# Optimization experiments

Hardware: AMD Instinct MI355X
Metric: run time of the kernel (lower is better)

The kernel has to match this reference:

```python
import jax, jax.numpy as jnp
import numpy as np

WIN = 9
PAD = WIN // 2
ALPHA = 0.1
BETA = 0.1
EPS_NCC = 1e-5
EPS_SC = 1e-5


def box_sum(x):
    """All-ones WIN^3 box-filter local sum, stride 1, pad WIN//2.
    Implemented separably (3 1-D convs) -- mathematically identical to the
    original single F.conv3d with a ones [1,1,9,9,9] kernel, far cheaper.
    x: [N, 1, D, H, W]"""
    for axis in range(3):
        kshape = [1, 1, 1, 1, 1]
        kshape[2 + axis] = WIN
        kern = jnp.ones(kshape, x.dtype)
        pad = [(0, 0), (0, 0), (0, 0)]
        pad[axis] = (PAD, PAD)
        x = jax.lax.conv_general_dilated(x, kern, (1, 1, 1), pad)
    return x


def setup_inputs() -> dict:
    key = jax.random.key(0)
    k1, k2, k3, k4, k5 = jax.random.split(key, 5)
    B, T, D, H, W = 1, 4, 128, 128, 128
    image = jax.random.normal(k1, (B, T, D, H, W), jnp.float32)
    mask = jax.random.uniform(k2, (B, T, D, H, W), jnp.float32)
    pred_image = jax.random.normal(k3, (B, T, D, H, W), jnp.float32)
    pred_mask = jax.random.uniform(k4, (B, T, D, H, W), jnp.float32)
    flow = jax.random.normal(k5, (T - 1, B, 3, D, H, W), jnp.float32)
    time_diff = jnp.arange(B * T, dtype=jnp.float32).reshape(B, T)
    return {"image": image, "mask": mask, "pred_image": pred_image,
            "pred_mask": pred_mask, "flow": flow, "time_diff": time_diff}


def reference(image, mask, pred_image, pred_mask, flow, time_diff):
    B, T, D, H, W = image.shape
    win_size = WIN ** 3

    # ---- NCC loss: fixed frame (t=0) vs each predicted frame t=1..T-1 ----
    # Per-t (1 - mean(cc_t)) averaged over T-1 equals 1 - mean over the
    # stacked batch since every cc_t has identical shape.
    I = jnp.broadcast_to(image[:, :1], (B, T - 1, D, H, W)).reshape(B * (T - 1), 1, D, H, W)
    J = pred_image[:, 1:].reshape(B * (T - 1), 1, D, H, W)
    I_sum = box_sum(I)
    J_sum = box_sum(J)
    I2_sum = box_sum(I * I)
    J2_sum = box_sum(J * J)
    IJ_sum = box_sum(I * J)
    u_I = I_sum / win_size
    u_J = J_sum / win_size
    cross = IJ_sum - u_J * I_sum - u_I * J_sum + u_I * u_J * win_size
    I_var = I2_sum - 2 * u_I * I_sum + u_I * u_I * win_size
    J_var = J2_sum - 2 * u_J * J_sum + u_J * u_J * win_size
    cc = cross * cross / (I_var * J_var + EPS_NCC)
    ncc = 1.0 - jnp.mean(cc)

    # ---- gradient (flow smoothness) loss, l2 penalty ----
    # flow: [T-1, B, 3, D, H, W]; per-t means of equal-shaped diffs average
    # to the global mean over the leading t axis.
    dy = jnp.square(jnp.abs(flow[:, :, :, 1:, :, :] - flow[:, :, :, :-1, :, :]))
    dx = jnp.square(jnp.abs(flow[:, :, :, :, 1:, :] - flow[:, :, :, :, :-1, :]))
    dz = jnp.square(jnp.abs(flow[:, :, :, :, :, 1:] - flow[:, :, :, :, :, :-1]))
    grad_loss = (jnp.mean(dx) + jnp.mean(dy) + jnp.mean(dz)) / 3.0

    # ---- temporal volume smoothness constraint ----
    area = jnp.sum(pred_mask, axis=(2, 3, 4)).T  # [T, B]
    area = area / jnp.max(area)
    scs = []
    for i in range(T - 2):
        for j in range(i + 1, T - 1):
            for k in range(j + 1, T):
                lam = (time_diff[:, j] - time_diff[:, i] + EPS_SC) / (
                    time_diff[:, k] - time_diff[:, i] + EPS_SC)
                scs.append(jnp.square(area[j] - area[i] - lam * (area[k] - area[i])))
    sc = jnp.mean(jnp.stack(scs, axis=1))

    return ncc + ALPHA * grad_loss + BETA * sc
```

## Files before the change

kernel.cpp:

```cpp
#include <hip/hip_runtime.h>

#define V3 (128 * 128 * 128)

__device__ __forceinline__ float block_reduce(float v, float* sm) {
#pragma unroll
  for (int off = 32; off > 0; off >>= 1) v += __shfl_down(v, off, 64);
  int lane = threadIdx.x & 63;
  int wid  = threadIdx.x >> 6;
  if (lane == 0) sm[wid] = v;
  __syncthreads();
  float r = 0.f;
  if ((int)threadIdx.x < (int)(blockDim.x >> 6)) r = sm[threadIdx.x];
  if (wid == 0) {
#pragma unroll
    for (int off = 4; off > 0; off >>= 1) r += __shfl_down(r, off, 64);
  }
  __syncthreads();
  return r;
}

__global__ __launch_bounds__(256) void area_kernel(const float* __restrict__ pm,
                                                   float* __restrict__ acc) {
  __shared__ float sm[8];
  const int t = blockIdx.y;
  const float* p = pm + (size_t)t * V3;
  const int n4 = V3 / 4;
  float s = 0.f;
  for (int i = blockIdx.x * blockDim.x + threadIdx.x; i < n4;
       i += gridDim.x * blockDim.x) {
    float4 a = *(const float4*)(p + 4 * (size_t)i);
    s += (a.x + a.y) + (a.z + a.w);
  }
  s = block_reduce(s, sm);
  if (threadIdx.x == 0) atomicAdd(acc + t, s);
}

__global__ __launch_bounds__(256) void grad_kernel(const float* __restrict__ fl,
                                                   float* __restrict__ acc) {
  __shared__ float sm[8];
  const int w4 = threadIdx.x & 31;
  const int hl = threadIdx.x >> 5;
  const int h  = blockIdx.x * 8 + hl;
  const int d0 = blockIdx.y * 16;
  const int c  = blockIdx.z;
  const float* p = fl + (size_t)c * V3 + (size_t)h * 128 + w4 * 4;
  const bool hv = (h < 127);

  float s = 0.f;
  float4 cur  = *(const float4*)(p + (size_t)d0 * 16384);
  float4 curh = hv ? *(const float4*)(p + (size_t)d0 * 16384 + 128) : cur;

#pragma unroll
  for (int dd = 0; dd < 16; ++dd) {
    const int d = d0 + dd;
    const bool dv = (d < 127);
    float4 nxt = cur, nxth = curh;
    if (dv) {
      nxt = *(const float4*)(p + (size_t)(d + 1) * 16384);
      if (hv) nxth = *(const float4*)(p + (size_t)(d + 1) * 16384 + 128);
    }
    float x;
    x = cur.y - cur.x; s += x * x;
    x = cur.z - cur.y; s += x * x;
    x = cur.w - cur.z; s += x * x;
    float nx = __shfl_down(cur.x, 1, 64);
    if (w4 != 31) { x = nx - cur.w; s += x * x; }
    if (hv) {
      x = curh.x - cur.x; s += x * x;
      x = curh.y - cur.y; s += x * x;
      x = curh.z - cur.z; s += x * x;
      x = curh.w - cur.w; s += x * x;
    }
    if (dv) {
      x = nxt.x - cur.x; s += x * x;
      x = nxt.y - cur.y; s += x * x;
      x = nxt.z - cur.z; s += x * x;
      x = nxt.w - cur.w; s += x * x;
    }
    cur = nxt; curh = nxth;
  }
  s = block_reduce(s, sm);
  if (threadIdx.x == 0) atomicAdd(acc, s);
}

template <bool WITH_I>
__global__ __launch_bounds__(256) void n1_kernel(const float* __restrict__ I0,
                                                 const float* __restrict__ Jall,
                                                 float* __restrict__ FI,
                                                 float* __restrict__ FJall) {
  constexpr int NF = WITH_I ? 5 : 3;
  __shared__ float sI[2][2][136];
  __shared__ float sJ[2][2][136];
  __shared__ float ring[2][9][NF][128];

  const int tz = blockIdx.z;
  const float* J = Jall + (size_t)tz * V3;
  float* FJ = FJall + (size_t)tz * 3 * (size_t)V3;

  const int w  = threadIdx.x & 127;
  const int dl = threadIdx.x >> 7;
  const int d  = blockIdx.y * 2 + dl;
  const int h0 = blockIdx.x * 16;
  const float* Ib = I0 + (size_t)d * 16384;
  const float* Jb = J  + (size_t)d * 16384;

#pragma unroll
  for (int sl = 0; sl < 9; ++sl)
#pragma unroll
    for (int f = 0; f < NF; ++f) ring[dl][sl][f][w] = 0.f;

  float S[NF];
#pragma unroll
  for (int f = 0; f < NF; ++f) S[f] = 0.f;

  for (int hh = h0 - 4; hh < h0 + 20; ++hh) {
    const int buf = hh & 1;
    const bool valid = (hh >= 0) && (hh < 128);
    if (valid) {
      sI[dl][buf][4 + w] = Ib[hh * 128 + w];
      sJ[dl][buf][4 + w] = Jb[hh * 128 + w];
      if (w < 4)    { sI[dl][buf][w] = 0.f;     sJ[dl][buf][w] = 0.f; }
      if (w >= 124) { sI[dl][buf][w + 8] = 0.f; sJ[dl][buf][w + 8] = 0.f; }
    }
    __syncthreads();

    float Wn[NF];
#pragma unroll
    for (int f = 0; f < NF; ++f) Wn[f] = 0.f;
    if (valid) {
#pragma unroll
      for (int k = 0; k < 9; ++k) {
        float a = sI[dl][buf][w + k];
        float b = sJ[dl][buf][w + k];
        if (WITH_I) {
          Wn[0] += a; Wn[1] += a * a;
          Wn[2] += b; Wn[3] += b * b; Wn[4] += a * b;
        } else {
          Wn[0] += b; Wn[1] += b * b; Wn[2] += a * b;
        }
      }
    }

    const int slot = (hh + 36) % 9;
#pragma unroll
    for (int f = 0; f < NF; ++f) {
      float old = ring[dl][slot][f][w];
      ring[dl][slot][f][w] = Wn[f];
      S[f] += Wn[f] - old;
    }

    const int ho = hh - 4;
    if (ho >= h0) {
      size_t base = (size_t)d * 16384 + (size_t)ho * 128 + w;
      if (WITH_I) {
        FI[base]                  = S[0];
        FI[(size_t)V3 + base]     = S[1];
        FJ[base]                  = S[2];
        FJ[(size_t)V3 + base]     = S[3];
        FJ[2 * (size_t)V3 + base] = S[4];
      } else {
        FJ[base]                  = S[0];
        FJ[(size_t)V3 + base]     = S[1];
        FJ[2 * (size_t)V3 + base] = S[2];
      }
    }
  }
}

__global__ __launch_bounds__(256) void n2_kernel(const float* __restrict__ FI,
                                                 const float* __restrict__ FJall,
                                                 float* __restrict__ acc) {
  __shared__ float sm[8];
  const float* FJ = FJall + (size_t)blockIdx.z * 3 * (size_t)V3;
  const int w  = threadIdx.x & 127;
  const int h  = blockIdx.x * 2 + (threadIdx.x >> 7);
  const int d0 = blockIdx.y * 16;
  const int hw = h * 128 + w;

  const float* P0 = FI;
  const float* P1 = FI + (size_t)V3;
  const float* P2 = FJ;
  const float* P3 = FJ + (size_t)V3;
  const float* P4 = FJ + 2 * (size_t)V3;

  float S0 = 0.f, S1 = 0.f, S2 = 0.f, S3 = 0.f, S4 = 0.f;
#pragma unroll
  for (int k = 0; k < 9; ++k) {
    int dd = d0 - 4 + k;
    bool v = (dd >= 0) && (dd < 128);
    size_t a = (size_t)(v ? dd : 0) * 16384 + hw;
    S0 += v ? P0[a] : 0.f;
    S1 += v ? P1[a] : 0.f;
    S2 += v ? P2[a] : 0.f;
    S3 += v ? P3[a] : 0.f;
    S4 += v ? P4[a] : 0.f;
  }

  const float inv_win = 1.0f / 729.0f;
  float accv = 0.f;
#pragma unroll 4
  for (int d = d0; d < d0 + 16; ++d) {
    float cross = S4 - S0 * S2 * inv_win;
    float Ivar  = S1 - S0 * S0 * inv_win;
    float Jvar  = S3 - S2 * S2 * inv_win;
    accv += cross * cross / (Ivar * Jvar + 1e-5f);

    int da = d + 5, ds = d - 4;
    bool va = da < 128, vs = ds >= 0;
    size_t aa = (size_t)(va ? da : 0) * 16384 + hw;
    size_t as = (size_t)(vs ? ds : 0) * 16384 + hw;
    S0 += (va ? P0[aa] : 0.f) - (vs ? P0[as] : 0.f);
    S1 += (va ? P1[aa] : 0.f) - (vs ? P1[as] : 0.f);
    S2 += (va ? P2[aa] : 0.f) - (vs ? P2[as] : 0.f);
    S3 += (va ? P3[aa] : 0.f) - (vs ? P3[as] : 0.f);
    S4 += (va ? P4[aa] : 0.f) - (vs ? P4[as] : 0.f);
  }

  accv = block_reduce(accv, sm);
  if (threadIdx.x == 0) atomicAdd(acc, accv);
}

__global__ void final_kernel(const float* __restrict__ ws,
                             const float* __restrict__ td,
                             float* __restrict__ out) {
  if (threadIdx.x != 0 || blockIdx.x != 0) return;
  float area[4];
  float amax = -1e30f;
#pragma unroll
  for (int t = 0; t < 4; ++t) {
    area[t] = ws[t];
    amax = fmaxf(amax, area[t]);
  }
  float a[4];
#pragma unroll
  for (int t = 0; t < 4; ++t) a[t] = area[t] / amax;

  float sc = 0.f;
  int cnt = 0;
  for (int i = 0; i < 2; ++i)
    for (int j = i + 1; j < 3; ++j)
      for (int k = j + 1; k < 4; ++k) {
        float lam = (td[j] - td[i] + 1e-5f) / (td[k] - td[i] + 1e-5f);
        float e = a[j] - a[i] - lam * (a[k] - a[i]);
        sc += e * e;
        ++cnt;
      }
  sc /= (float)cnt;

  float ncc  = 1.0f - ws[7] / (3.0f * (float)V3);
  float grad = ws[4] / (3.0f * 9.0f * 127.0f * 128.0f * 128.0f);
  out[0] = ncc + 0.1f * grad + 0.1f * sc;
}

extern "C" void kernel_launch(void* const* d_in, const int* in_sizes, int n_in,
                              void* d_out, int out_size, void* d_ws, size_t ws_size,
                              hipStream_t stream) {
  const float* image      = (const float*)d_in[0];
  const float* pred_image = (const float*)d_in[2];
  const float* pred_mask  = (const float*)d_in[3];
  const float* flow       = (const float*)d_in[4];
  const float* time_diff  = (const float*)d_in[5];
  float* out = (float*)d_out;
  float* wsf = (float*)d_ws;
  float* FI  = wsf + 64;
  float* FJ  = FI + 2 * (size_t)V3;

  hipMemsetAsync(d_ws, 0, 256, stream);

  hipLaunchKernelGGL(area_kernel, dim3(512, 4), dim3(256), 0, stream,
                     pred_mask, wsf);
  hipLaunchKernelGGL(grad_kernel, dim3(16, 8, 9), dim3(256), 0, stream,
                     flow, wsf + 4);

  const size_t need_fused = (64 + 11 * (size_t)V3) * sizeof(float);
  if (ws_size >= need_fused) {
    hipLaunchKernelGGL((n1_kernel<true>), dim3(8, 64, 1), dim3(256), 0, stream,
                       image, pred_image + (size_t)V3, FI, FJ);
    hipLaunchKernelGGL((n1_kernel<false>), dim3(8, 64, 2), dim3(256), 0, stream,
                       image, pred_image + 2 * (size_t)V3, FI,
                       FJ + 3 * (size_t)V3);
    hipLaunchKernelGGL(n2_kernel, dim3(64, 8, 3), dim3(256), 0, stream,
                       FI, FJ, wsf + 7);
  } else {
    for (int t = 0; t < 3; ++t) {
      const float* J = pred_image + (size_t)(t + 1) * V3;
      if (t == 0) {
        hipLaunchKernelGGL((n1_kernel<true>), dim3(8, 64, 1), dim3(256), 0,
                           stream, image, J, FI, FJ);
      } else {
        hipLaunchKernelGGL((n1_kernel<false>), dim3(8, 64, 1), dim3(256), 0,
                           stream, image, J, FI, FJ);
      }
      hipLaunchKernelGGL(n2_kernel, dim3(64, 8, 1), dim3(256), 0, stream,
                         FI, FJ, wsf + 7);
    }
  }

  hipLaunchKernelGGL(final_kernel, dim3(1), dim3(1), 0, stream,
                     wsf, time_diff, out);
}
```

Measured before the change: 154.0 us.

## Vectorize NCC box-sum passes and double-buffer row staging with smaller tiles

```diff
diff --git a/kernel.cpp b/kernel.cpp
--- a/kernel.cpp
+++ b/kernel.cpp
@@ -16,6 +16,15 @@
     for (int off = 4; off > 0; off >>= 1) r += __shfl_down(r, off, 64);
   }
   __syncthreads();
+  return r;
+}
+
+__device__ __forceinline__ float4 ldz(const float* __restrict__ p, size_t off,
+                                      bool v) {
+  const float4 q = *(const float4*)(p + off);
+  float4 r;
+  r.x = v ? q.x : 0.f; r.y = v ? q.y : 0.f;
+  r.z = v ? q.z : 0.f; r.w = v ? q.w : 0.f;
   return r;
 }
 
@@ -100,29 +109,49 @@
   const int w  = threadIdx.x & 127;
   const int dl = threadIdx.x >> 7;
   const int d  = blockIdx.y * 2 + dl;
-  const int h0 = blockIdx.x * 16;
+  const int h0 = blockIdx.x * 8;
   const float* Ib = I0 + (size_t)d * 16384;
   const float* Jb = J  + (size_t)d * 16384;
 
+  if (w < 4) {
+    sI[dl][0][w] = 0.f; sI[dl][1][w] = 0.f;
+    sJ[dl][0][w] = 0.f; sJ[dl][1][w] = 0.f;
+  }
+  if (w >= 124) {
+    sI[dl][0][w + 8] = 0.f; sI[dl][1][w + 8] = 0.f;
+    sJ[dl][0][w + 8] = 0.f; sJ[dl][1][w + 8] = 0.f;
+  }
 #pragma unroll
   for (int sl = 0; sl < 9; ++sl)
 #pragma unroll
     for (int f = 0; f < NF; ++f) ring[dl][sl][f][w] = 0.f;
 
+  auto stage = [&](int hh) {
+    if (hh >= 0 && hh < 128) {
+      const int b = hh & 1;
+      if (w < 32) {
+        float4 v = *(const float4*)(Ib + hh * 128 + w * 4);
+        *(float4*)&sI[dl][b][4 + w * 4] = v;
+      } else if (w < 64) {
+        const int l = w - 32;
+        float4 v = *(const float4*)(Jb + hh * 128 + l * 4);
+        *(float4*)&sJ[dl][b][4 + l * 4] = v;
+      }
+    }
+  };
+
   float S[NF];
 #pragma unroll
   for (int f = 0; f < NF; ++f) S[f] = 0.f;
 
-  for (int hh = h0 - 4; hh < h0 + 20; ++hh) {
-    const int buf = hh & 1;
+  stage(h0 - 4);
+  int slot = (h0 + 32) % 9;
+
+  for (int hh = h0 - 4; hh < h0 + 12; ++hh) {
+    __syncthreads();
+    stage(hh + 1);
+    const int b = hh & 1;
     const bool valid = (hh >= 0) && (hh < 128);
-    if (valid) {
-      sI[dl][buf][4 + w] = Ib[hh * 128 + w];
-      sJ[dl][buf][4 + w] = Jb[hh * 128 + w];
-      if (w < 4)    { sI[dl][buf][w] = 0.f;     sJ[dl][buf][w] = 0.f; }
-      if (w >= 124) { sI[dl][buf][w + 8] = 0.f; sJ[dl][buf][w + 8] = 0.f; }
-    }
-    __syncthreads();
 
     float Wn[NF];
 #pragma unroll
@@ -130,24 +159,24 @@
     if (valid) {
 #pragma unroll
       for (int k = 0; k < 9; ++k) {
-        float a = sI[dl][buf][w + k];
-        float b = sJ[dl][buf][w + k];
+        float a = sI[dl][b][w + k];
+        float bb = sJ[dl][b][w + k];
         if (WITH_I) {
           Wn[0] += a; Wn[1] += a * a;
-          Wn[2] += b; Wn[3] += b * b; Wn[4] += a * b;
+          Wn[2] += bb; Wn[3] += bb * bb; Wn[4] += a * bb;
         } else {
-          Wn[0] += b; Wn[1] += b * b; Wn[2] += a * b;
+          Wn[0] += bb; Wn[1] += bb * bb; Wn[2] += a * bb;
         }
       }
     }
 
-    const int slot = (hh + 36) % 9;
 #pragma unroll
     for (int f = 0; f < NF; ++f) {
       float old = ring[dl][slot][f][w];
       ring[dl][slot][f][w] = Wn[f];
       S[f] += Wn[f] - old;
     }
+    ++slot; if (slot == 9) slot = 0;
 
     const int ho = hh - 4;
     if (ho >= h0) {
@@ -172,10 +201,10 @@
                                                  float* __restrict__ acc) {
   __shared__ float sm[8];
   const float* FJ = FJall + (size_t)blockIdx.z * 3 * (size_t)V3;
-  const int w  = threadIdx.x & 127;
-  const int h  = blockIdx.x * 2 + (threadIdx.x >> 7);
-  const int d0 = blockIdx.y * 16;
-  const int hw = h * 128 + w;
+  const int w4 = threadIdx.x & 31;
+  const int h  = blockIdx.x * 8 + (threadIdx.x >> 5);
+  const int d0 = blockIdx.y * 8;
+  const size_t hw = (size_t)h * 128 + w4 * 4;
 
   const float* P0 = FI;
   const float* P1 = FI + (size_t)V3;
@@ -183,37 +212,60 @@
   const float* P3 = FJ + (size_t)V3;
   const float* P4 = FJ + 2 * (size_t)V3;
 
-  float S0 = 0.f, S1 = 0.f, S2 = 0.f, S3 = 0.f, S4 = 0.f;
+  float4 S0 = {0,0,0,0}, S1 = {0,0,0,0}, S2 = {0,0,0,0},
+         S3 = {0,0,0,0}, S4 = {0,0,0,0};
 #pragma unroll
   for (int k = 0; k < 9; ++k) {
     int dd = d0 - 4 + k;
     bool v = (dd >= 0) && (dd < 128);
     size_t a = (size_t)(v ? dd : 0) * 16384 + hw;
-    S0 += v ? P0[a] : 0.f;
-    S1 += v ? P1[a] : 0.f;
-    S2 += v ? P2[a] : 0.f;
-    S3 += v ? P3[a] : 0.f;
-    S4 += v ? P4[a] : 0.f;
+    float4 q;
+    q = ldz(P0, a, v); S0.x += q.x; S0.y += q.y; S0.z += q.z; S0.w += q.w;
+    q = ldz(P1, a, v); S1.x += q.x; S1.y += q.y; S1.z += q.z; S1.w += q.w;
+    q = ldz(P2, a, v); S2.x += q.x; S2.y += q.y; S2.z += q.z; S2.w += q.w;
+    q = ldz(P3, a, v); S3.x += q.x; S3.y += q.y; S3.z += q.z; S3.w += q.w;
+    q = ldz(P4, a, v); S4.x += q.x; S4.y += q.y; S4.z += q.z; S4.w += q.w;
   }
 
   const float inv_win = 1.0f / 729.0f;
   float accv = 0.f;
-#pragma unroll 4
-  for (int d = d0; d < d0 + 16; ++d) {
-    float cross = S4 - S0 * S2 * inv_win;
-    float Ivar  = S1 - S0 * S0 * inv_win;
-    float Jvar  = S3 - S2 * S2 * inv_win;
-    accv += cross * cross / (Ivar * Jvar + 1e-5f);
-
-    int da = d + 5, ds = d - 4;
-    bool va = da < 128, vs = ds >= 0;
-    size_t aa = (size_t)(va ? da : 0) * 16384 + hw;
-    size_t as = (size_t)(vs ? ds : 0) * 16384 + hw;
-    S0 += (va ? P0[aa] : 0.f) - (vs ? P0[as] : 0.f);
-    S1 += (va ? P1[aa] : 0.f) - (vs ? P1[as] : 0.f);
-    S2 += (va ? P2[aa] : 0.f) - (vs ? P2[as] : 0.f);
-    S3 += (va ? P3[aa] : 0.f) - (vs ? P3[as] : 0.f);
-    S4 += (va ? P4[aa] : 0.f) - (vs ? P4[as] : 0.f);
+#pragma unroll
+  for (int dd = 0; dd < 8; ++dd) {
+    const int d = d0 + dd;
+    {
+      float c0, iv, jv;
+      c0 = S4.x - S0.x * S2.x * inv_win;
+      iv = S1.x - S0.x * S0.x * inv_win;
+      jv = S3.x - S2.x * S2.x * inv_win;
+      accv += c0 * c0 * __builtin_amdgcn_rcpf(iv * jv + 1e-5f);
+      c0 = S4.y - S0.y * S2.y * inv_win;
+      iv = S1.y - S0.y * S0.y * inv_win;
+      jv = S3.y - S2.y * S2.y * inv_win;
+      accv += c0 * c0 * __builtin_amdgcn_rcpf(iv * jv + 1e-5f);
+      c0 = S4.z - S0.z * S2.z * inv_win;
+      iv = S1.z - S0.z * S0.z * inv_win;
+      jv = S3.z - S2.z * S2.z * inv_win;
+      accv += c0 * c0 * __builtin_amdgcn_rcpf(iv * jv + 1e-5f);
+      c0 = S4.w - S0.w * S2.w * inv_win;
+      iv = S1.w - S0.w * S0.w * inv_win;
+      jv = S3.w - S2.w * S2.w * inv_win;
+      accv += c0 * c0 * __builtin_amdgcn_rcpf(iv * jv + 1e-5f);
+    }
+    const int da = d + 5, ds = d - 4;
+    const bool va = da < 128, vs = ds >= 0;
+    const size_t aa = (size_t)(va ? da : 0) * 16384 + hw;
+    const size_t as = (size_t)(vs ? ds : 0) * 16384 + hw;
+    float4 q, r;
+    q = ldz(P0, aa, va); r = ldz(P0, as, vs);
+    S0.x += q.x - r.x; S0.y += q.y - r.y; S0.z += q.z - r.z; S0.w += q.w - r.w;
+    q = ldz(P1, aa, va); r = ldz(P1, as, vs);
+    S1.x += q.x - r.x; S1.y += q.y - r.y; S1.z += q.z - r.z; S1.w += q.w - r.w;
+    q = ldz(P2, aa, va); r = ldz(P2, as, vs);
+    S2.x += q.x - r.x; S2.y += q.y - r.y; S2.z += q.z - r.z; S2.w += q.w - r.w;
+    q = ldz(P3, aa, va); r = ldz(P3, as, vs);
+    S3.x += q.x - r.x; S3.y += q.y - r.y; S3.z += q.z - r.z; S3.w += q.w - r.w;
+    q = ldz(P4, aa, va); r = ldz(P4, as, vs);
+    S4.x += q.x - r.x; S4.y += q.y - r.y; S4.z += q.z - r.z; S4.w += q.w - r.w;
   }
 
   accv = block_reduce(accv, sm);
@@ -274,24 +326,24 @@
 
   const size_t need_fused = (64 + 11 * (size_t)V3) * sizeof(float);
   if (ws_size >= need_fused) {
-    hipLaunchKernelGGL((n1_kernel<true>), dim3(8, 64, 1), dim3(256), 0, stream,
+    hipLaunchKernelGGL((n1_kernel<true>), dim3(16, 64, 1), dim3(256), 0, stream,
                        image, pred_image + (size_t)V3, FI, FJ);
-    hipLaunchKernelGGL((n1_kernel<false>), dim3(8, 64, 2), dim3(256), 0, stream,
+    hipLaunchKernelGGL((n1_kernel<false>), dim3(16, 64, 2), dim3(256), 0, stream,
                        image, pred_image + 2 * (size_t)V3, FI,
                        FJ + 3 * (size_t)V3);
-    hipLaunchKernelGGL(n2_kernel, dim3(64, 8, 3), dim3(256), 0, stream,
+    hipLaunchKernelGGL(n2_kernel, dim3(16, 16, 3), dim3(256), 0, stream,
                        FI, FJ, wsf + 7);
   } else {
     for (int t = 0; t < 3; ++t) {
       const float* J = pred_image + (size_t)(t + 1) * V3;
       if (t == 0) {
-        hipLaunchKernelGGL((n1_kernel<true>), dim3(8, 64, 1), dim3(256), 0,
+        hipLaunchKernelGGL((n1_kernel<true>), dim3(16, 64, 1), dim3(256), 0,
                            stream, image, J, FI, FJ);
       } else {
-        hipLaunchKernelGGL((n1_kernel<false>), dim3(8, 64, 1), dim3(256), 0,
+        hipLaunchKernelGGL((n1_kernel<false>), dim3(16, 64, 1), dim3(256), 0,
                            stream, image, J, FI, FJ);
       }
-      hipLaunchKernelGGL(n2_kernel, dim3(64, 8, 1), dim3(256), 0, stream,
+      hipLaunchKernelGGL(n2_kernel, dim3(16, 16, 1), dim3(256), 0, stream,
                          FI, FJ, wsf + 7);
     }
   }
```

After: 157.8 us. 2.5% more time.
